# Optimization experiments

Measured on AMD Instinct MI355X. Metric: run time of the kernel, lower is better.

## Reference

```python
import jax, jax.numpy as jnp
import numpy as np
import math

B, S, D_IN, D_OUT, H = 2, 2048, 1024, 1024, 16
HD = D_OUT // H


def setup_inputs() -> dict:
    key = jax.random.key(0)
    ks = jax.random.split(key, 6)
    scale = 0.02
    return {
        "x": jax.random.normal(ks[0], (B, S, D_IN), dtype=jnp.float32),
        "Wq": jax.random.normal(ks[1], (D_IN, D_OUT), dtype=jnp.float32) * scale,
        "Wk": jax.random.normal(ks[2], (D_IN, D_OUT), dtype=jnp.float32) * scale,
        "Wv": jax.random.normal(ks[3], (D_IN, D_OUT), dtype=jnp.float32) * scale,
        "Wo": jax.random.normal(ks[4], (D_OUT, D_OUT), dtype=jnp.float32) * scale,
        "bo": jax.random.normal(ks[5], (D_OUT,), dtype=jnp.float32) * scale,
    }


def reference(x, Wq, Wk, Wv, Wo, bo):
    b, n, _ = x.shape
    # project and split heads -> [b, h, n, hd]
    q = (x @ Wq).reshape(b, n, H, HD).transpose(0, 2, 1, 3)
    k = (x @ Wk).reshape(b, n, H, HD).transpose(0, 2, 1, 3)
    v = (x @ Wv).reshape(b, n, H, HD).transpose(0, 2, 1, 3)
    # materialized [b, h, n, n] scores with causal mask (as in original)
    scores = jnp.einsum('bhqd,bhkd->bhqk', q, k)
    causal = jnp.tril(jnp.ones((n, n), dtype=bool))  # True = keep
    scores = jnp.where(causal, scores, -jnp.inf)
    attn = jax.nn.softmax(scores / math.sqrt(HD), axis=-1)
    ctx = jnp.einsum('bhqk,bhkd->bhqd', attn, v)
    ctx = ctx.transpose(0, 2, 1, 3).reshape(b, n, D_OUT)
    return ctx @ Wo + bo
```

## Files before the change

kernel.cpp:

```cpp
#include <hip/hip_runtime.h>
#include <hip/hip_bf16.h>
#include <math.h>

typedef __bf16 v8bf __attribute__((ext_vector_type(8)));
typedef float  v4f  __attribute__((ext_vector_type(4)));
typedef unsigned short u16;

static_assert(sizeof(v8bf) == 16, "v8bf must be 16B");

__device__ __forceinline__ u16 f2bf(float f) {
  __hip_bfloat16 h = __float2bfloat16(f);
  return *reinterpret_cast<u16*>(&h);
}
__device__ __forceinline__ v4f mfma16(v8bf a, v8bf b, v4f c) {
  return __builtin_amdgcn_mfma_f32_16x16x32_bf16(a, b, c, 0, 0, 0);
}
__device__ __forceinline__ void async16(const u16* g, u16* l) {
  __builtin_amdgcn_global_load_lds(
      (__attribute__((address_space(1))) void*)(void*)g,
      (__attribute__((address_space(3))) void*)l, 16, 0, 0);
}

__global__ void prep(const float* __restrict__ x, const float* __restrict__ Wq,
                     const float* __restrict__ Wk, const float* __restrict__ Wv,
                     const float* __restrict__ Wo, u16* __restrict__ Wt,
                     u16* __restrict__ xb) {
  int tx = threadIdx.x, ty = threadIdx.y;
  if (blockIdx.z == 4) {
    int bid = blockIdx.y * 32 + blockIdx.x;
    int i = (bid * 1024 + ty * 32 + tx) * 4;
    float4 v = *(const float4*)(x + i);
    ushort4 o;
    o.x = f2bf(v.x); o.y = f2bf(v.y); o.z = f2bf(v.z); o.w = f2bf(v.w);
    *(ushort4*)(xb + i) = o;
    return;
  }
  __shared__ float tile[32][33];
  const float* src = (blockIdx.z == 0) ? Wq : (blockIdx.z == 1) ? Wk : (blockIdx.z == 2) ? Wv : Wo;
  int k0 = blockIdx.x * 32, n0 = blockIdx.y * 32;
  tile[ty][tx] = src[(size_t)(k0 + ty) * 1024 + n0 + tx];
  __syncthreads();
  Wt[(size_t)(blockIdx.z * 1024 + n0 + ty) * 1024 + k0 + tx] = f2bf(tile[tx][ty]);
}

__device__ __forceinline__ void gemm_core(const u16* __restrict__ A, const u16* __restrict__ Bt,
                                          u16* sA, u16* sB, v4f acc[4][4], int bm, int bn) {
  const int t = threadIdx.x;
  const int w = t >> 6, l = t & 63;
  const int quad = l >> 4, low = l & 15;
  const int wm = (w & 1) * 64, wn = (w >> 1) * 64;
  const int rowA = bm * 128 + w * 32 + (l >> 2);
  const int rowB = bn * 128 + w * 32 + (l >> 2);
  const int col8 = (l & 3) * 8;
  u16* la = sA + w * 1024;
  u16* lb = sB + w * 1024;

  for (int kb = 0; kb < 1024; kb += 32) {
    async16(A + (size_t)rowA * 1024 + kb + col8, la);
    async16(A + (size_t)(rowA + 16) * 1024 + kb + col8, la + 512);
    async16(Bt + (size_t)rowB * 1024 + kb + col8, lb);
    async16(Bt + (size_t)(rowB + 16) * 1024 + kb + col8, lb + 512);
    __syncthreads();
    v8bf af[4], bfr[4];
#pragma unroll
    for (int i = 0; i < 4; i++)
      af[i] = *(const v8bf*)(sA + (wm + i * 16 + low) * 32 + quad * 8);
#pragma unroll
    for (int j = 0; j < 4; j++)
      bfr[j] = *(const v8bf*)(sB + (wn + j * 16 + low) * 32 + quad * 8);
#pragma unroll
    for (int i = 0; i < 4; i++)
#pragma unroll
      for (int j = 0; j < 4; j++)
        acc[i][j] = mfma16(af[i], bfr[j], acc[i][j]);
    __syncthreads();
  }
}

__global__ __launch_bounds__(256) void gemm_qkv(const u16* __restrict__ xb,
                                                const u16* __restrict__ Wt,
                                                u16* __restrict__ Qb,
                                                u16* __restrict__ Kb,
                                                u16* __restrict__ Vt) {
  __shared__ __align__(16) u16 sA[128 * 32];
  __shared__ __align__(16) u16 sB[128 * 32];
  v4f acc[4][4] = {};
  const int bm = blockIdx.x, bn = blockIdx.y;
  gemm_core(xb, Wt, sA, sB, acc, bm, bn);
  const int t = threadIdx.x, w = t >> 6, l = t & 63, quad = l >> 4, low = l & 15;
  const int wm = (w & 1) * 64, wn = (w >> 1) * 64;
  const int zone = (bn * 128) >> 10;
  const float qsc = (zone == 0) ? 0.18033688011112042f : 1.0f;
#pragma unroll
  for (int i = 0; i < 4; i++) {
    int m0 = bm * 128 + wm + i * 16 + quad * 4;
#pragma unroll
    for (int j = 0; j < 4; j++) {
      int nn = (bn * 128 + wn + j * 16 + low) & 1023;
      if (zone == 0) {
#pragma unroll
        for (int r = 0; r < 4; r++)
          Qb[(size_t)(m0 + r) * 1024 + nn] = f2bf(acc[i][j][r] * qsc);
      } else if (zone == 1) {
#pragma unroll
        for (int r = 0; r < 4; r++)
          Kb[(size_t)(m0 + r) * 1024 + nn] = f2bf(acc[i][j][r]);
      } else {
        int bb = m0 >> 11, s = m0 & 2047;
#pragma unroll
        for (int r = 0; r < 4; r++)
          Vt[(size_t)(bb * 1024 + nn) * 2048 + s + r] = f2bf(acc[i][j][r]);
      }
    }
  }
}

__global__ __launch_bounds__(256) void gemm_out(const u16* __restrict__ ctx,
                                                const u16* __restrict__ Wt,
                                                const float* __restrict__ bo,
                                                float* __restrict__ out) {
  __shared__ __align__(16) u16 sA[128 * 32];
  __shared__ __align__(16) u16 sB[64 * 32];
  const u16* Bt = Wt + (size_t)3072 * 1024;
  v4f acc[4][2] = {};
  const int bm = blockIdx.x, bn = blockIdx.y;
  const int t = threadIdx.x, w = t >> 6, l = t & 63, quad = l >> 4, low = l & 15;
  const int wm = (w & 1) * 64, wn = (w >> 1) * 32;
  const int rowA = bm * 128 + w * 32 + (l >> 2);
  const int rowB = bn * 64 + w * 16 + (l >> 2);
  const int col8 = (l & 3) * 8;
  u16* la = sA + w * 1024;
  u16* lb = sB + w * 512;

  for (int kb = 0; kb < 1024; kb += 32) {
    async16(ctx + (size_t)rowA * 1024 + kb + col8, la);
    async16(ctx + (size_t)(rowA + 16) * 1024 + kb + col8, la + 512);
    async16(Bt + (size_t)rowB * 1024 + kb + col8, lb);
    __syncthreads();
    v8bf af[4], bfr[2];
#pragma unroll
    for (int i = 0; i < 4; i++)
      af[i] = *(const v8bf*)(sA + (wm + i * 16 + low) * 32 + quad * 8);
#pragma unroll
    for (int j = 0; j < 2; j++)
      bfr[j] = *(const v8bf*)(sB + (wn + j * 16 + low) * 32 + quad * 8);
#pragma unroll
    for (int i = 0; i < 4; i++)
#pragma unroll
      for (int j = 0; j < 2; j++)
        acc[i][j] = mfma16(af[i], bfr[j], acc[i][j]);
    __syncthreads();
  }
#pragma unroll
  for (int i = 0; i < 4; i++) {
    int m0 = bm * 128 + wm + i * 16 + quad * 4;
#pragma unroll
    for (int j = 0; j < 2; j++) {
      int n = bn * 64 + wn + j * 16 + low;
      float bias = bo[n];
#pragma unroll
      for (int r = 0; r < 4; r++)
        out[(size_t)(m0 + r) * 1024 + n] = acc[i][j][r] + bias;
    }
  }
}

__global__ __launch_bounds__(256) void attn(const u16* __restrict__ Qb,
                                            const u16* __restrict__ Kb,
                                            const u16* __restrict__ Vt,
                                            u16* __restrict__ ctx) {
  __shared__ __align__(16) u16 sK[2][4096];
  __shared__ __align__(16) u16 sV[2][4096];
  __shared__ __align__(16) u16 pS[4][32][72];
  const int t = threadIdx.x, w = t >> 6, l = t & 63, quad = l >> 4, low = l & 15;
  const int h = blockIdx.x, tile = 15 - blockIdx.y, b = blockIdx.z;
  const int qw = tile * 128 + w * 32;
  const int nkt = 2 * tile + 2;

  const u16* kbase = Kb + (size_t)(b * 2048) * 1024 + h * 64;
  const u16* vbase = Vt + (size_t)(b * 1024 + h * 64) * 2048;

  const int srow = l >> 3;
  const int cg = (l & 7) ^ srow;

  v8bf qa[2][2];
#pragma unroll
  for (int mi = 0; mi < 2; mi++) {
    const u16* qrow = Qb + (size_t)(b * 2048 + qw + mi * 16 + low) * 1024 + h * 64;
    qa[mi][0] = *(const v8bf*)(qrow + quad * 8);
    qa[mi][1] = *(const v8bf*)(qrow + 32 + quad * 8);
  }

  float li[2][4] = {};
  v4f o[2][4] = {};

  {
    const u16* kg = kbase + (size_t)(w * 8 + srow) * 1024 + cg * 8;
    async16(kg, &sK[0][w * 512]);
    async16(kg + (size_t)32 * 1024, &sK[0][2048 + w * 512]);
    const u16* vg = vbase + (size_t)(w * 8 + srow) * 2048 + cg * 8;
    async16(vg, &sV[0][w * 512]);
    async16(vg + (size_t)32 * 2048, &sV[0][2048 + w * 512]);
  }

  for (int it = 0; it < nkt; it++) {
    __syncthreads();
    const int kb = it * 64;
    const int cur = it & 1;
    if (it + 1 < nkt) {
      const int nb = (it + 1) & 1;
      const u16* kg = kbase + (size_t)(kb + 64 + w * 8 + srow) * 1024 + cg * 8;
      async16(kg, &sK[nb][w * 512]);
      async16(kg + (size_t)32 * 1024, &sK[nb][2048 + w * 512]);
      const u16* vg = vbase + (size_t)(w * 8 + srow) * 2048 + kb + 64 + cg * 8;
      async16(vg, &sV[nb][w * 512]);
      async16(vg + (size_t)32 * 2048, &sV[nb][2048 + w * 512]);
    }

    const bool active = (kb <= qw + 31);
    if (active) {
      v4f s[2][4] = {};
#pragma unroll
      for (int cf = 0; cf < 4; cf++) {
        const int key = cf * 16 + low;
        v8bf kf0 = *(const v8bf*)(&sK[cur][key * 64 + ((quad ^ (key & 7)) * 8)]);
        v8bf kf1 = *(const v8bf*)(&sK[cur][key * 64 + (((4 + quad) ^ (key & 7)) * 8)]);
#pragma unroll
        for (int mi = 0; mi < 2; mi++) {
          s[mi][cf] = mfma16(qa[mi][0], kf0, s[mi][cf]);
          s[mi][cf] = mfma16(qa[mi][1], kf1, s[mi][cf]);
        }
      }

      const bool dm = (kb + 63 > qw);
#pragma unroll
      for (int mi = 0; mi < 2; mi++)
#pragma unroll
        for (int r = 0; r < 4; r++) {
          const int qr = qw + mi * 16 + quad * 4 + r;
#pragma unroll
          for (int cf = 0; cf < 4; cf++) {
            float e = __builtin_amdgcn_exp2f(s[mi][cf][r]);
            if (dm && (kb + cf * 16 + low > qr)) e = 0.f;
            li[mi][r] += e;
            pS[w][mi * 16 + quad * 4 + r][cf * 16 + low] = f2bf(e);
          }
        }

      v8bf pa[2][2];
#pragma unroll
      for (int mi = 0; mi < 2; mi++) {
        pa[mi][0] = *(const v8bf*)(&pS[w][mi * 16 + low][quad * 8]);
        pa[mi][1] = *(const v8bf*)(&pS[w][mi * 16 + low][32 + quad * 8]);
      }
#pragma unroll
      for (int df = 0; df < 4; df++) {
        const int d = df * 16 + low;
        v8bf vf0 = *(const v8bf*)(&sV[cur][d * 64 + ((quad ^ (d & 7)) * 8)]);
        v8bf vf1 = *(const v8bf*)(&sV[cur][d * 64 + (((4 + quad) ^ (d & 7)) * 8)]);
#pragma unroll
        for (int mi = 0; mi < 2; mi++) {
          o[mi][df] = mfma16(pa[mi][0], vf0, o[mi][df]);
          o[mi][df] = mfma16(pa[mi][1], vf1, o[mi][df]);
        }
      }
    }
  }

#pragma unroll
  for (int off = 1; off < 16; off <<= 1)
#pragma unroll
    for (int mi = 0; mi < 2; mi++)
#pragma unroll
      for (int r = 0; r < 4; r++)
        li[mi][r] += __shfl_xor(li[mi][r], off);

#pragma unroll
  for (int mi = 0; mi < 2; mi++)
#pragma unroll
    for (int r = 0; r < 4; r++) {
      float inv = 1.f / li[mi][r];
      int row = b * 2048 + qw + mi * 16 + quad * 4 + r;
#pragma unroll
      for (int df = 0; df < 4; df++)
        ctx[(size_t)row * 1024 + h * 64 + df * 16 + low] = f2bf(o[mi][df][r] * inv);
    }
}

extern "C" void kernel_launch(void* const* d_in, const int* in_sizes, int n_in,
                              void* d_out, int out_size, void* d_ws, size_t ws_size,
                              hipStream_t stream) {
  const float* x  = (const float*)d_in[0];
  const float* Wq = (const float*)d_in[1];
  const float* Wk = (const float*)d_in[2];
  const float* Wv = (const float*)d_in[3];
  const float* Wo = (const float*)d_in[4];
  const float* bo = (const float*)d_in[5];
  float* out = (float*)d_out;

  char* ws = (char*)d_ws;
  u16* xb  = (u16*)(ws);
  u16* Wt  = (u16*)(ws + 8ull * 1024 * 1024);
  u16* Qb  = (u16*)(ws + 16ull * 1024 * 1024);
  u16* Kb  = (u16*)(ws + 24ull * 1024 * 1024);
  u16* Vt  = (u16*)(ws + 32ull * 1024 * 1024);
  u16* ctx = (u16*)(ws + 40ull * 1024 * 1024);

  prep<<<dim3(32, 32, 5), dim3(32, 32, 1), 0, stream>>>(x, Wq, Wk, Wv, Wo, Wt, xb);
  gemm_qkv<<<dim3(32, 24, 1), dim3(256, 1, 1), 0, stream>>>(xb, Wt, Qb, Kb, Vt);
  attn<<<dim3(16, 16, 2), dim3(256, 1, 1), 0, stream>>>(Qb, Kb, Vt, ctx);
  gemm_out<<<dim3(32, 16, 1), dim3(256, 1, 1), 0, stream>>>(ctx, Wt, bo, out);
}
```

Before: 205.5 us.

## Keep attention probabilities in registers via transposed S and 16x16x16 MFMA

The attention kernel now computes S transposed (K as the A operand, Q as B), so each lane's accumulator already matches the A-operand layout of a 16x16x16 bf16 MFMA. P can then feed the PV MFMA straight from registers, which removes the LDS staging buffer pS and its write/read round trip. The query tile shrinks from 128 to 64 rows (16 per wave) and the grid doubles, so more blocks run with less causal waste per block. The cost is that each K/V tile is reused by half as many queries, so K/V global traffic doubles, and the PV step uses the smaller-K MFMA.

```diff
diff --git a/kernel.cpp b/kernel.cpp
--- a/kernel.cpp
+++ b/kernel.cpp
@@ -3,6 +3,8 @@
 #include <math.h>
 
 typedef __bf16 v8bf __attribute__((ext_vector_type(8)));
+typedef __bf16 v4bf __attribute__((ext_vector_type(4)));
+typedef short  v4s  __attribute__((ext_vector_type(4)));
 typedef float  v4f  __attribute__((ext_vector_type(4)));
 typedef unsigned short u16;
 
@@ -14,6 +16,15 @@
 }
 __device__ __forceinline__ v4f mfma16(v8bf a, v8bf b, v4f c) {
   return __builtin_amdgcn_mfma_f32_16x16x32_bf16(a, b, c, 0, 0, 0);
+}
+__device__ __forceinline__ v4f mfma16k16(v4bf a, v4bf b, v4f c) {
+#if __has_builtin(__builtin_amdgcn_mfma_f32_16x16x16_bf16)
+  return __builtin_amdgcn_mfma_f32_16x16x16_bf16(a, b, c, 0, 0, 0);
+#else
+  union { v4bf f; v4s s; } ua, ub;
+  ua.f = a; ub.f = b;
+  return __builtin_amdgcn_mfma_f32_16x16x16bf16_1k(ua.s, ub.s, c, 0, 0, 0);
+#endif
 }
 __device__ __forceinline__ void async16(const u16* g, u16* l) {
   __builtin_amdgcn_global_load_lds(
@@ -171,11 +182,10 @@
                                             u16* __restrict__ ctx) {
   __shared__ __align__(16) u16 sK[2][4096];
   __shared__ __align__(16) u16 sV[2][4096];
-  __shared__ __align__(16) u16 pS[4][32][72];
   const int t = threadIdx.x, w = t >> 6, l = t & 63, quad = l >> 4, low = l & 15;
-  const int h = blockIdx.x, tile = 15 - blockIdx.y, b = blockIdx.z;
-  const int qw = tile * 128 + w * 32;
-  const int nkt = 2 * tile + 2;
+  const int h = blockIdx.x, tile = 31 - blockIdx.y, b = blockIdx.z;
+  const int qw = tile * 64 + w * 16;
+  const int nkt = tile + 1;
 
   const u16* kbase = Kb + (size_t)(b * 2048) * 1024 + h * 64;
   const u16* vbase = Vt + (size_t)(b * 1024 + h * 64) * 2048;
@@ -183,16 +193,12 @@
   const int srow = l >> 3;
   const int cg = (l & 7) ^ srow;
 
-  v8bf qa[2][2];
-#pragma unroll
-  for (int mi = 0; mi < 2; mi++) {
-    const u16* qrow = Qb + (size_t)(b * 2048 + qw + mi * 16 + low) * 1024 + h * 64;
-    qa[mi][0] = *(const v8bf*)(qrow + quad * 8);
-    qa[mi][1] = *(const v8bf*)(qrow + 32 + quad * 8);
-  }
-
-  float li[2][4] = {};
-  v4f o[2][4] = {};
+  const u16* qrow_p = Qb + (size_t)(b * 2048 + qw + low) * 1024 + h * 64;
+  v8bf qa0 = *(const v8bf*)(qrow_p + quad * 8);
+  v8bf qa1 = *(const v8bf*)(qrow_p + 32 + quad * 8);
+
+  float li = 0.f;
+  v4f o[4] = {};
 
   {
     const u16* kg = kbase + (size_t)(w * 8 + srow) * 1024 + cg * 8;
@@ -217,74 +223,53 @@
       async16(vg + (size_t)32 * 2048, &sV[nb][2048 + w * 512]);
     }
 
-    const bool active = (kb <= qw + 31);
-    if (active) {
-      v4f s[2][4] = {};
+    v4f s[4] = {};
+#pragma unroll
+    for (int cf = 0; cf < 4; cf++) {
+      const int key = cf * 16 + low;
+      v8bf kf0 = *(const v8bf*)(&sK[cur][key * 64 + ((quad ^ (key & 7)) * 8)]);
+      v8bf kf1 = *(const v8bf*)(&sK[cur][key * 64 + (((4 + quad) ^ (key & 7)) * 8)]);
+      s[cf] = mfma16(kf0, qa0, s[cf]);
+      s[cf] = mfma16(kf1, qa1, s[cf]);
+    }
+
+    const bool dm = (it == nkt - 1);
+    const int qr = qw + low;
+    v4bf pf[4];
+#pragma unroll
+    for (int cf = 0; cf < 4; cf++)
+#pragma unroll
+      for (int r = 0; r < 4; r++) {
+        float e = __builtin_amdgcn_exp2f(s[cf][r]);
+        if (dm && (kb + cf * 16 + quad * 4 + r > qr)) e = 0.f;
+        li += e;
+        pf[cf][r] = (__bf16)e;
+      }
+
+#pragma unroll
+    for (int df = 0; df < 4; df++) {
+      const int d = df * 16 + low;
 #pragma unroll
       for (int cf = 0; cf < 4; cf++) {
-        const int key = cf * 16 + low;
-        v8bf kf0 = *(const v8bf*)(&sK[cur][key * 64 + ((quad ^ (key & 7)) * 8)]);
-        v8bf kf1 = *(const v8bf*)(&sK[cur][key * 64 + (((4 + quad) ^ (key & 7)) * 8)]);
-#pragma unroll
-        for (int mi = 0; mi < 2; mi++) {
-          s[mi][cf] = mfma16(qa[mi][0], kf0, s[mi][cf]);
-          s[mi][cf] = mfma16(qa[mi][1], kf1, s[mi][cf]);
-        }
+        const int c = cf * 2 + (quad >> 1);
+        const v4bf vf = *(const v4bf*)(&sV[cur][d * 64 + ((c ^ (d & 7)) * 8) + (quad & 1) * 4]);
+        o[df] = mfma16k16(pf[cf], vf, o[df]);
       }
-
-      const bool dm = (kb + 63 > qw);
-#pragma unroll
-      for (int mi = 0; mi < 2; mi++)
-#pragma unroll
-        for (int r = 0; r < 4; r++) {
-          const int qr = qw + mi * 16 + quad * 4 + r;
-#pragma unroll
-          for (int cf = 0; cf < 4; cf++) {
-            float e = __builtin_amdgcn_exp2f(s[mi][cf][r]);
-            if (dm && (kb + cf * 16 + low > qr)) e = 0.f;
-            li[mi][r] += e;
-            pS[w][mi * 16 + quad * 4 + r][cf * 16 + low] = f2bf(e);
-          }
-        }
-
-      v8bf pa[2][2];
-#pragma unroll
-      for (int mi = 0; mi < 2; mi++) {
-        pa[mi][0] = *(const v8bf*)(&pS[w][mi * 16 + low][quad * 8]);
-        pa[mi][1] = *(const v8bf*)(&pS[w][mi * 16 + low][32 + quad * 8]);
-      }
-#pragma unroll
-      for (int df = 0; df < 4; df++) {
-        const int d = df * 16 + low;
-        v8bf vf0 = *(const v8bf*)(&sV[cur][d * 64 + ((quad ^ (d & 7)) * 8)]);
-        v8bf vf1 = *(const v8bf*)(&sV[cur][d * 64 + (((4 + quad) ^ (d & 7)) * 8)]);
-#pragma unroll
-        for (int mi = 0; mi < 2; mi++) {
-          o[mi][df] = mfma16(pa[mi][0], vf0, o[mi][df]);
-          o[mi][df] = mfma16(pa[mi][1], vf1, o[mi][df]);
-        }
-      }
-    }
-  }
-
-#pragma unroll
-  for (int off = 1; off < 16; off <<= 1)
-#pragma unroll
-    for (int mi = 0; mi < 2; mi++)
-#pragma unroll
-      for (int r = 0; r < 4; r++)
-        li[mi][r] += __shfl_xor(li[mi][r], off);
-
-#pragma unroll
-  for (int mi = 0; mi < 2; mi++)
-#pragma unroll
-    for (int r = 0; r < 4; r++) {
-      float inv = 1.f / li[mi][r];
-      int row = b * 2048 + qw + mi * 16 + quad * 4 + r;
-#pragma unroll
-      for (int df = 0; df < 4; df++)
-        ctx[(size_t)row * 1024 + h * 64 + df * 16 + low] = f2bf(o[mi][df][r] * inv);
-    }
+    }
+  }
+
+  li += __shfl_xor(li, 16);
+  li += __shfl_xor(li, 32);
+
+#pragma unroll
+  for (int r = 0; r < 4; r++) {
+    float lir = __shfl(li, quad * 4 + r);
+    float inv = 1.f / lir;
+    int row = b * 2048 + qw + quad * 4 + r;
+#pragma unroll
+    for (int df = 0; df < 4; df++)
+      ctx[(size_t)row * 1024 + h * 64 + df * 16 + low] = f2bf(o[df][r] * inv);
+  }
 }
 
 extern "C" void kernel_launch(void* const* d_in, const int* in_sizes, int n_in,
@@ -308,6 +293,6 @@
 
   prep<<<dim3(32, 32, 5), dim3(32, 32, 1), 0, stream>>>(x, Wq, Wk, Wv, Wo, Wt, xb);
   gemm_qkv<<<dim3(32, 24, 1), dim3(256, 1, 1), 0, stream>>>(xb, Wt, Qb, Kb, Vt);
-  attn<<<dim3(16, 16, 2), dim3(256, 1, 1), 0, stream>>>(Qb, Kb, Vt, ctx);
+  attn<<<dim3(16, 32, 2), dim3(256, 1, 1), 0, stream>>>(Qb, Kb, Vt, ctx);
   gemm_out<<<dim3(32, 16, 1), dim3(256, 1, 1), 0, stream>>>(ctx, Wt, bo, out);
 }
```

After: 175.6 us. 1.17x faster.
